# Performance work log

Measured on AMD Instinct MI355X. Metric: run time of the kernel, lower is better.

The kernel has to match this reference:

```python
import jax, jax.numpy as jnp
import numpy as np

ODE_UNFOLDS = 6          # kerasncp LTCCell default
EPS = 1e-8               # kerasncp LTCCell epsilon


def _masks(d):
    """Adjacency masks from MemoryCellWiring: self-synapses on all 2d units,
    cross synapses src<->src+d (polarity -1); sensory src->src and src->src+d
    (polarity +1)."""
    units = 2 * d
    m = np.eye(units, dtype=np.float32)
    m[:d, d:] += np.eye(d, dtype=np.float32)
    m[d:, :d] += np.eye(d, dtype=np.float32)
    sm = np.zeros((d, units), dtype=np.float32)
    sm[:, :d] = np.eye(d, dtype=np.float32)
    sm[:, d:] = np.eye(d, dtype=np.float32)
    return jnp.asarray(m), jnp.asarray(sm)


def setup_inputs() -> dict:
    key = jax.random.key(0)
    B, T, d = 32, 128, 128
    units = 2 * d
    ks = jax.random.split(key, 12)
    U = lambda k, shp, lo, hi: jax.random.uniform(k, shp, jnp.float32, lo, hi)
    mask, smask = _masks(d)
    return {
        "inputs": jax.random.normal(ks[0], (B, T, d), jnp.float32),
        # affine input/output mappings (kerasncp init: ones / zeros)
        "input_w": jnp.ones((d,), jnp.float32),
        "input_b": jnp.zeros((d,), jnp.float32),
        "output_w": jnp.ones((d,), jnp.float32),
        "output_b": jnp.zeros((d,), jnp.float32),
        # per-neuron params (kerasncp init ranges)
        "gleak": U(ks[1], (units,), 0.001, 1.0),
        "vleak": U(ks[2], (units,), -0.2, 0.2),
        "cm": U(ks[3], (units,), 0.4, 0.6),
        # recurrent synapse params (units, units); erev initialized to polarity
        "w": U(ks[4], (units, units), 0.001, 1.0),
        "mu": U(ks[5], (units, units), 0.3, 0.8),
        "sigma": U(ks[6], (units, units), 3.0, 8.0),
        "erev": -mask,
        # sensory synapse params (d, units); polarity +1
        "sensory_w": U(ks[7], (d, units), 0.001, 1.0),
        "sensory_mu": U(ks[8], (d, units), 0.3, 0.8),
        "sensory_sigma": U(ks[9], (d, units), 3.0, 8.0),
        "sensory_erev": smask,
    }


def reference(inputs, input_w, input_b, output_w, output_b,
              gleak, vleak, cm, w, mu, sigma, erev,
              sensory_w, sensory_mu, sensory_sigma, sensory_erev):
    B, T, d = inputs.shape
    units = 2 * d
    mask, smask = _masks(d)
    x = inputs * input_w + input_b          # affine input mapping, (B,T,d)
    cm_t = cm * ODE_UNFOLDS                  # cm / (elapsed_time / ode_unfolds), elapsed=1

    def step(v, x_t):
        # sensory activations, computed once per timestep: (B, d, units)
        sa = sensory_w * jax.nn.sigmoid((x_t[:, :, None] - sensory_mu) * sensory_sigma) * smask
        wnum_s = jnp.sum(sa * sensory_erev, axis=1)   # (B, units)
        wden_s = jnp.sum(sa, axis=1)                  # (B, units)

        def unfold(v, _):
            # semi-implicit Euler fixed-point step; (B, units, units)
            wa = w * jax.nn.sigmoid((v[:, :, None] - mu) * sigma) * mask
            num = cm_t * v + gleak * vleak + jnp.sum(wa * erev, axis=1) + wnum_s
            den = cm_t + gleak + jnp.sum(wa, axis=1) + wden_s
            return num / (den + EPS), None

        v, _ = jax.lax.scan(unfold, v, None, length=ODE_UNFOLDS)
        return v, None

    v0 = jnp.zeros((B, units), inputs.dtype)
    vT, _ = jax.lax.scan(step, v0, jnp.swapaxes(x, 0, 1))
    # motor neurons = first output_dim = d units, then affine output mapping
    return vT[:, :d] * output_w + output_b
```

## Files before the change

kernel.cpp:

```cpp
#include <hip/hip_runtime.h>

#define ODE_UNFOLDS 6
#define LTC_EPS 1e-8f


__device__ __forceinline__ float swap_pair(float x) {
    return __int_as_float(
        __builtin_amdgcn_mov_dpp(__float_as_int(x), 0xB1, 0xF, 0xF, true));
}

struct Base { float db, nbdb, K0, Ks, Kx; };

__global__ __launch_bounds__(64)
void ltc_lane_kernel(const float* __restrict__ inputs,
                     const float* __restrict__ input_w, const float* __restrict__ input_b,
                     const float* __restrict__ output_w, const float* __restrict__ output_b,
                     const float* __restrict__ gleak, const float* __restrict__ vleak,
                     const float* __restrict__ cm,
                     const float* __restrict__ w, const float* __restrict__ mu,
                     const float* __restrict__ sigma, const float* __restrict__ erev,
                     const float* __restrict__ sw, const float* __restrict__ smu,
                     const float* __restrict__ ssig, const float* __restrict__ serev,
                     float* __restrict__ out,
                     int B, int T, int d)
{
    const int tid = blockIdx.x * blockDim.x + threadIdx.x;
    const int units = 2 * d;
    if (tid >= B * units) return;

    const int pairIdx = tid >> 1;
    const int h = tid & 1;
    const int b = pairIdx / d;
    const int j = pairIdx - b * d;
    const int u  = j + h * d;
    const int pu = j + (1 - h) * d;

    const float LOG2E = 1.4426950408889634f;

    float A_s, C_s, W_s;
    {
        int i = u * units + u;
        float sg = sigma[i], m = mu[i];
        A_s = -sg * LOG2E; C_s = m * sg * LOG2E;
        W_s = w[i] * (-erev[i]);
    }
    float W_c;
    {
        int i = pu * units + u;
        W_c = w[i] * (-erev[i]);
    }
    float A_o, C_o;
    {
        int i = u * units + pu;
        float sg = sigma[i], m = mu[i];
        A_o = -sg * LOG2E; C_o = m * sg * LOG2E;
    }
    const float Wsum = W_s + W_c;

    float siA, siC, sW;
    {
        int i = j * units + u;
        float sg = ssig[i], m = smu[i];
        float sA = -sg * LOG2E, sC = m * sg * LOG2E;
        const float iw = input_w[j], ib = input_b[j];
        siA = iw * sA; siC = ib * sA + sC;
        sW = sw[i] * serev[i];
    }

    const float cmu = cm[u] * (float)ODE_UNFOLDS;
    const float gl  = gleak[u];
    const float gv  = gl * vleak[u];
    const float den0 = cmu + gl + LTC_EPS;
    const float sW2 = 2.f * sW;
    const float gvden0 = gv + den0;

    const float* __restrict__ xin = inputs + (size_t)b * T * d + j;

    auto make_base = [&](float x) -> Base {
        const float e  = __builtin_amdgcn_exp2f(fmaf(x, siA, siC));
        const float ss = __builtin_amdgcn_rcpf(1.f + e);
        Base bb;
        bb.db   = fmaf(sW,  ss, den0);
        bb.nbdb = fmaf(sW2, ss, gvden0);
        bb.K0 = bb.db + Wsum;
        bb.Ks = bb.db + W_c;
        bb.Kx = bb.db + W_s;
        return bb;
    };

    float num = 0.f, r = 1.f;

    const int TU = 4;
    float xbuf[TU];
#pragma unroll
    for (int k = 0; k < TU; ++k) xbuf[k] = xin[(size_t)k * d];

    Base cur = make_base(xbuf[0]);

    for (int g = 0; g < T; g += TU) {
        float xnext[TU];
        if (g + TU < T) {
#pragma unroll
            for (int k = 0; k < TU; ++k) xnext[k] = xin[(size_t)(g + TU + k) * d];
        } else {
#pragma unroll
            for (int k = 0; k < TU; ++k) xnext[k] = 0.f;
        }

#pragma unroll
        for (int k = 0; k < TU; ++k) {
            const float xn1 = (k + 1 < TU) ? xbuf[k + 1] : xnext[0];
            const Base nxt = make_base(xn1);

#pragma unroll
            for (int uu = 0; uu < ODE_UNFOLDS; ++uu) {
                const float cn = cmu * num;
                const float ts = A_s * num;
                const float to = A_o * num;
                const float argo = fmaf(to, r, C_o);
                const float args = fmaf(ts, r, C_s);
                const float eo = __builtin_amdgcn_exp2f(argo);
                const float es = __builtin_amdgcn_exp2f(args);
                const float ex = swap_pair(eo);

                const float tdb = fmaf(cn, r, cur.nbdb);
                const float pe  = 1.f + es;
                const float P1  = fmaf(cur.Ks, es, cur.K0);
                const float P2  = fmaf(cur.db, es, cur.Kx);
                const float Pp  = fmaf(pe, ex, pe);
                const float den = fmaf(P2, ex, P1);

                num = fmaf(tdb, Pp, -den);
                r   = __builtin_amdgcn_rcpf(den);
            }

            cur = nxt;
        }

#pragma unroll
        for (int k = 0; k < TU; ++k) xbuf[k] = xnext[k];
    }

    if (h == 0) {
        const float v = num * r;
        out[(size_t)b * d + j] = fmaf(v, output_w[j], output_b[j]);
    }
}

extern "C" void kernel_launch(void* const* d_in, const int* in_sizes, int n_in,
                              void* d_out, int out_size, void* d_ws, size_t ws_size,
                              hipStream_t stream) {
    const float* inputs   = (const float*)d_in[0];
    const float* input_w  = (const float*)d_in[1];
    const float* input_b  = (const float*)d_in[2];
    const float* output_w = (const float*)d_in[3];
    const float* output_b = (const float*)d_in[4];
    const float* gleak    = (const float*)d_in[5];
    const float* vleak    = (const float*)d_in[6];
    const float* cm       = (const float*)d_in[7];
    const float* w        = (const float*)d_in[8];
    const float* mu       = (const float*)d_in[9];
    const float* sigma    = (const float*)d_in[10];
    const float* erev     = (const float*)d_in[11];
    const float* sw       = (const float*)d_in[12];
    const float* smu      = (const float*)d_in[13];
    const float* ssig     = (const float*)d_in[14];
    const float* serev    = (const float*)d_in[15];
    float* out = (float*)d_out;

    const int d = in_sizes[1];
    const int B = out_size / d;
    const int T = in_sizes[0] / (B * d);

    const int total = B * 2 * d;
    const int block = 64;
    const int grid = (total + block - 1) / block;
    ltc_lane_kernel<<<grid, block, 0, stream>>>(
        inputs, input_w, input_b, output_w, output_b,
        gleak, vleak, cm, w, mu, sigma, erev,
        sw, smu, ssig, serev, out, B, T, d);
}
```

Measured before the change: 36.52 us.

## Process two batch rows per thread using packed float2 math

Each thread now carries two independent batch recurrences (b and b+B/2) using 2-wide vector types so the compiler can emit packed FMA/mul instructions, halving the thread count. The goal is to add instruction-level parallelism to the serial latency-bound recurrence and use packed FP32 ops. Transcendentals stay scalar, and the grid shrinks to half the waves, which may leave CUs idle on a device with many CUs. For odd B the second row is clamped and written twice.

```diff
diff --git a/kernel.cpp b/kernel.cpp
--- a/kernel.cpp
+++ b/kernel.cpp
@@ -3,16 +3,18 @@
 #define ODE_UNFOLDS 6
 #define LTC_EPS 1e-8f
 
+
+typedef float v2f __attribute__((ext_vector_type(2)));
 
 __device__ __forceinline__ float swap_pair(float x) {
     return __int_as_float(
         __builtin_amdgcn_mov_dpp(__float_as_int(x), 0xB1, 0xF, 0xF, true));
 }
 
-struct Base { float db, nbdb, K0, Ks, Kx; };
+struct Base2 { v2f db, nbdb, K0, Ks, Kx; };
 
 __global__ __launch_bounds__(64)
-void ltc_lane_kernel(const float* __restrict__ inputs,
+void ltc_twin_kernel(const float* __restrict__ inputs,
                      const float* __restrict__ input_w, const float* __restrict__ input_b,
                      const float* __restrict__ output_w, const float* __restrict__ output_b,
                      const float* __restrict__ gleak, const float* __restrict__ vleak,
@@ -24,14 +26,16 @@
                      float* __restrict__ out,
                      int B, int T, int d)
 {
+    const int Bh = (B + 1) >> 1;
+    const int units = 2 * d;
     const int tid = blockIdx.x * blockDim.x + threadIdx.x;
-    const int units = 2 * d;
-    if (tid >= B * units) return;
+    if (tid >= Bh * units) return;
 
     const int pairIdx = tid >> 1;
     const int h = tid & 1;
-    const int b = pairIdx / d;
-    const int j = pairIdx - b * d;
+    const int b1 = pairIdx / d;
+    const int j  = pairIdx - b1 * d;
+    int b2 = b1 + Bh; if (b2 >= B) b2 = B - 1;
     const int u  = j + h * d;
     const int pu = j + (1 - h) * d;
 
@@ -74,76 +78,97 @@
     const float sW2 = 2.f * sW;
     const float gvden0 = gv + den0;
 
-    const float* __restrict__ xin = inputs + (size_t)b * T * d + j;
-
-    auto make_base = [&](float x) -> Base {
-        const float e  = __builtin_amdgcn_exp2f(fmaf(x, siA, siC));
-        const float ss = __builtin_amdgcn_rcpf(1.f + e);
-        Base bb;
-        bb.db   = fmaf(sW,  ss, den0);
-        bb.nbdb = fmaf(sW2, ss, gvden0);
-        bb.K0 = bb.db + Wsum;
-        bb.Ks = bb.db + W_c;
-        bb.Kx = bb.db + W_s;
+    const v2f cmuV = {cmu, cmu};
+    const v2f AsV = {A_s, A_s}, CsV = {C_s, C_s};
+    const v2f AoV = {A_o, A_o}, CoV = {C_o, C_o};
+
+    const float* __restrict__ xin1 = inputs + (size_t)b1 * T * d + j;
+    const float* __restrict__ xin2 = inputs + (size_t)b2 * T * d + j;
+
+    auto make_base = [&](float xa, float xb) -> Base2 {
+        const float ea = __builtin_amdgcn_exp2f(fmaf(xa, siA, siC));
+        const float eb = __builtin_amdgcn_exp2f(fmaf(xb, siA, siC));
+        const float sa = __builtin_amdgcn_rcpf(1.f + ea);
+        const float sb = __builtin_amdgcn_rcpf(1.f + eb);
+        const v2f ss = {sa, sb};
+        Base2 bb;
+        bb.db   = __builtin_elementwise_fma(v2f{sW, sW},  ss, v2f{den0, den0});
+        bb.nbdb = __builtin_elementwise_fma(v2f{sW2, sW2}, ss, v2f{gvden0, gvden0});
+        bb.K0 = bb.db + v2f{Wsum, Wsum};
+        bb.Ks = bb.db + v2f{W_c, W_c};
+        bb.Kx = bb.db + v2f{W_s, W_s};
         return bb;
     };
 
-    float num = 0.f, r = 1.f;
+    v2f num = {0.f, 0.f};
+    v2f r   = {1.f, 1.f};
 
     const int TU = 4;
-    float xbuf[TU];
-#pragma unroll
-    for (int k = 0; k < TU; ++k) xbuf[k] = xin[(size_t)k * d];
-
-    Base cur = make_base(xbuf[0]);
+    float xb1[TU], xb2[TU];
+#pragma unroll
+    for (int k = 0; k < TU; ++k) { xb1[k] = xin1[(size_t)k * d]; xb2[k] = xin2[(size_t)k * d]; }
+
+    Base2 cur = make_base(xb1[0], xb2[0]);
 
     for (int g = 0; g < T; g += TU) {
-        float xnext[TU];
+        float xn1[TU], xn2[TU];
         if (g + TU < T) {
 #pragma unroll
-            for (int k = 0; k < TU; ++k) xnext[k] = xin[(size_t)(g + TU + k) * d];
+            for (int k = 0; k < TU; ++k) {
+                xn1[k] = xin1[(size_t)(g + TU + k) * d];
+                xn2[k] = xin2[(size_t)(g + TU + k) * d];
+            }
         } else {
 #pragma unroll
-            for (int k = 0; k < TU; ++k) xnext[k] = 0.f;
+            for (int k = 0; k < TU; ++k) { xn1[k] = 0.f; xn2[k] = 0.f; }
         }
 
 #pragma unroll
         for (int k = 0; k < TU; ++k) {
-            const float xn1 = (k + 1 < TU) ? xbuf[k + 1] : xnext[0];
-            const Base nxt = make_base(xn1);
+            const float xa = (k + 1 < TU) ? xb1[k + 1] : xn1[0];
+            const float xb = (k + 1 < TU) ? xb2[k + 1] : xn2[0];
+            const Base2 nxt = make_base(xa, xb);
 
 #pragma unroll
             for (int uu = 0; uu < ODE_UNFOLDS; ++uu) {
-                const float cn = cmu * num;
-                const float ts = A_s * num;
-                const float to = A_o * num;
-                const float argo = fmaf(to, r, C_o);
-                const float args = fmaf(ts, r, C_s);
-                const float eo = __builtin_amdgcn_exp2f(argo);
-                const float es = __builtin_amdgcn_exp2f(args);
-                const float ex = swap_pair(eo);
-
-                const float tdb = fmaf(cn, r, cur.nbdb);
-                const float pe  = 1.f + es;
-                const float P1  = fmaf(cur.Ks, es, cur.K0);
-                const float P2  = fmaf(cur.db, es, cur.Kx);
-                const float Pp  = fmaf(pe, ex, pe);
-                const float den = fmaf(P2, ex, P1);
-
-                num = fmaf(tdb, Pp, -den);
-                r   = __builtin_amdgcn_rcpf(den);
+                const v2f cn = cmuV * num;
+                const v2f ts = AsV * num;
+                const v2f to = AoV * num;
+                const v2f argo = __builtin_elementwise_fma(to, r, CoV);
+                const v2f args = __builtin_elementwise_fma(ts, r, CsV);
+
+                const float eo0 = __builtin_amdgcn_exp2f(argo.x);
+                const float eo1 = __builtin_amdgcn_exp2f(argo.y);
+                const float es0 = __builtin_amdgcn_exp2f(args.x);
+                const float es1 = __builtin_amdgcn_exp2f(args.y);
+                const float ex0 = swap_pair(eo0);
+                const float ex1 = swap_pair(eo1);
+                const v2f es = {es0, es1};
+                const v2f ex = {ex0, ex1};
+
+                const v2f tdb = __builtin_elementwise_fma(cn, r, cur.nbdb);
+                const v2f pe  = es + v2f{1.f, 1.f};
+                const v2f P1  = __builtin_elementwise_fma(cur.Ks, es, cur.K0);
+                const v2f P2  = __builtin_elementwise_fma(cur.db, es, cur.Kx);
+                const v2f Pp  = __builtin_elementwise_fma(pe, ex, pe);
+                const v2f den = __builtin_elementwise_fma(P2, ex, P1);
+
+                num = __builtin_elementwise_fma(tdb, Pp, -den);
+                r.x = __builtin_amdgcn_rcpf(den.x);
+                r.y = __builtin_amdgcn_rcpf(den.y);
             }
 
             cur = nxt;
         }
 
 #pragma unroll
-        for (int k = 0; k < TU; ++k) xbuf[k] = xnext[k];
+        for (int k = 0; k < TU; ++k) { xb1[k] = xn1[k]; xb2[k] = xn2[k]; }
     }
 
     if (h == 0) {
-        const float v = num * r;
-        out[(size_t)b * d + j] = fmaf(v, output_w[j], output_b[j]);
+        const float ow = output_w[j], ob = output_b[j];
+        out[(size_t)b1 * d + j] = fmaf(num.x * r.x, ow, ob);
+        out[(size_t)b2 * d + j] = fmaf(num.y * r.y, ow, ob);
     }
 }
 
@@ -172,10 +197,11 @@
     const int B = out_size / d;
     const int T = in_sizes[0] / (B * d);
 
-    const int total = B * 2 * d;
+    const int Bh = (B + 1) >> 1;
+    const int total = Bh * 2 * d;
     const int block = 64;
     const int grid = (total + block - 1) / block;
-    ltc_lane_kernel<<<grid, block, 0, stream>>>(
+    ltc_twin_kernel<<<grid, block, 0, stream>>>(
         inputs, input_w, input_b, output_w, output_b,
         gleak, vleak, cm, w, mu, sigma, erev,
         sw, smu, ssig, serev, out, B, T, d);
```

Result: slower. 49.46 us (+35.4%).
